# Kernel tuning notes

Hardware: AMD Instinct MI355X
Metric: run time of the kernel (lower is better)

The kernel has to match this reference:

```python
import jax, jax.numpy as jnp
import numpy as np

B, F, Q = 8192, 128, 64
H1, H2 = 256, 256
THRESHOLD = 0.95
EPS = 1e-12


def setup_inputs() -> dict:
    key = jax.random.key(0)
    ks = jax.random.split(key, 8)
    in_dim = F + 1 + Q  # raw + quantum + graph feature
    def lin(k, fan_in, fan_out):
        bound = 1.0 / np.sqrt(fan_in)
        kw, kb = jax.random.split(k)
        W = jax.random.uniform(kw, (fan_out, fan_in), jnp.float32, -bound, bound)
        b = jax.random.uniform(kb, (fan_out,), jnp.float32, -bound, bound)
        return W, b
    W1, b1 = lin(ks[2], in_dim, H1)
    W2, b2 = lin(ks[3], H1, H2)
    W3, b3 = lin(ks[4], H2, 1)
    return {
        'x': jax.random.normal(ks[0], (B, F), jnp.float32),
        'quantum_features': jax.random.normal(ks[1], (B, Q), jnp.float32),
        'W1': W1, 'b1': b1, 'W2': W2, 'b2': b2, 'W3': W3, 'b3': b3,
    }


def _graph_feat(x):
    # normalized Gram matrix -> squared cosine fidelity -> threshold -> row mean
    xn = x / (jnp.linalg.norm(x, axis=1, keepdims=True) + EPS)  # [B, F]
    fid = jnp.square(xn @ xn.T)                                  # [B, B]
    adj = jnp.where(fid >= THRESHOLD, 1.0, 0.0)
    adj = adj * (1.0 - jnp.eye(x.shape[0], dtype=x.dtype))       # no self-edges
    return jnp.mean(adj, axis=1, keepdims=True)                  # [B, 1]


def reference(x, quantum_features, W1, b1, W2, b2, W3, b3):
    graph_feat = jax.lax.stop_gradient(_graph_feat(x))  # built under no_grad in torch
    feats = jnp.concatenate([x, quantum_features, graph_feat], axis=1)  # [B, F+Q+1]
    h = jax.nn.relu(feats @ W1.T + b1)
    h = jax.nn.relu(h @ W2.T + b2)
    out = h @ W3.T + b3  # [B, 1]
    return out[:, 0]
```

## Files before the change

kernel.cpp:

```cpp
#include <hip/hip_runtime.h>
#include <hip/hip_bf16.h>

typedef __attribute__((ext_vector_type(8))) short bf16x8;
typedef __attribute__((ext_vector_type(8))) int i32x8;
typedef __attribute__((ext_vector_type(4))) float f32x4;
typedef unsigned int uint;

#define NROWS 8192
#define F_DIM 128
#define Q_DIM 64
#define KPAD  224
#define H_DIM 256

static __device__ inline unsigned short bf_bits(__hip_bfloat16 b) {
  unsigned short u; __builtin_memcpy(&u, &b, 2); return u;
}
static __device__ inline uint packhl(float v) {
  __hip_bfloat16 h = __float2bfloat16(v);
  float hf = __bfloat162float(h);
  __hip_bfloat16 l = __float2bfloat16(v - hf);
  return ((uint)bf_bits(l) << 16) | (uint)bf_bits(h);
}

__global__ __launch_bounds__(256) void norm_prep_kernel(const float* __restrict__ x,
                                                        const float* __restrict__ q,
                                                        const float* __restrict__ W1,
                                                        const float* __restrict__ W2,
                                                        unsigned char* __restrict__ xn8,
                                                        uint* __restrict__ feats_p,
                                                        uint* __restrict__ W1P,
                                                        uint* __restrict__ W2P,
                                                        int* __restrict__ cnt) {
  int tid = threadIdx.x;
  if (blockIdx.x >= 2048) {
    int b = blockIdx.x - 2048;
    if (b < 256) {
      if (tid < KPAD) W1P[b * KPAD + tid] = (tid < 193) ? packhl(W1[b * 193 + tid]) : 0u;
    } else {
      int n = b - 256;
      W2P[n * 256 + tid] = packhl(W2[n * 256 + tid]);
    }
    return;
  }
  int lane = tid & 63;
  int row = blockIdx.x * 4 + (tid >> 6);
  if (blockIdx.x < 32) cnt[blockIdx.x * 256 + tid] = 0;
  const float2 v = *(const float2*)(x + (size_t)row * F_DIM + lane * 2);
  float s = v.x * v.x + v.y * v.y;
#pragma unroll
  for (int off = 32; off; off >>= 1) s += __shfl_xor(s, off);
  float inv = 1.0f / (sqrtf(s) + 1e-12f);
  int pk = __builtin_amdgcn_cvt_pk_fp8_f32(v.x * inv, v.y * inv, 0, 0);
  *(unsigned short*)(xn8 + (size_t)row * F_DIM + lane * 2) = (unsigned short)(pk & 0xffff);

  uint* frow = feats_p + (size_t)row * KPAD;
  uint2 u;
  u.x = packhl(v.x); u.y = packhl(v.y);
  *(uint2*)(frow + lane * 2) = u;
  if (lane < 32) {
    const float2 qv = *(const float2*)(q + (size_t)row * Q_DIM + lane * 2);
    u.x = packhl(qv.x); u.y = packhl(qv.y);
    *(uint2*)(frow + 128 + lane * 2) = u;
  } else if (lane < 48) {
    uint2 z = {0u, 0u};
    *(uint2*)(frow + 192 + (lane - 32) * 2) = z;
  }
}

__global__ __launch_bounds__(256) void gram8_kernel(const unsigned char* __restrict__ xn8,
                                                    int* __restrict__ cnt) {
  __shared__ char smem[32768];
  int tid = threadIdx.x;
  int lane = tid & 63;
  int wave = tid >> 6;
  int lr = lane & 15;
  int quad = lane >> 4;

  int t = blockIdx.x;
  int bi = (int)((129.0f - sqrtf(129.0f * 129.0f - 8.0f * (float)t)) * 0.5f);
  while ((bi + 1) * (129 - (bi + 1)) / 2 <= t) bi++;
  while (bi * (129 - bi) / 2 > t) bi--;
  int bj = bi + (t - bi * (129 - bi) / 2);
  int i0 = bi * 128, j0 = bj * 128;

#pragma unroll
  for (int it = 0; it < 8; ++it) {
    int half = it >> 2;
    int row = (it & 3) * 32 + (tid >> 3);
    int chunk = tid & 7;
    int grow = (half ? j0 : i0) + row;
    uint4 v = *(const uint4*)(xn8 + (size_t)grow * F_DIM + chunk * 16);
    *(uint4*)(smem + half * 16384 + row * 128 + ((chunk ^ (row & 7)) << 4)) = v;
  }
  __syncthreads();

  int wi = (wave >> 1) * 64, wj = (wave & 1) * 64;

  f32x4 acc[4][4];
#pragma unroll
  for (int i = 0; i < 4; i++)
#pragma unroll
    for (int j = 0; j < 4; j++) acc[i][j] = (f32x4){0.f, 0.f, 0.f, 0.f};

  i32x8 a[4], b[4];
#pragma unroll
  for (int tt = 0; tt < 4; tt++) {
    int r = wi + tt * 16 + lr;
    const char* base = smem + r * 128;
    uint4 lo = *(const uint4*)(base + (((2 * quad) ^ (r & 7)) << 4));
    uint4 hi = *(const uint4*)(base + (((2 * quad + 1) ^ (r & 7)) << 4));
    i32x8 f;
    f[0] = lo.x; f[1] = lo.y; f[2] = lo.z; f[3] = lo.w;
    f[4] = hi.x; f[5] = hi.y; f[6] = hi.z; f[7] = hi.w;
    a[tt] = f;
  }
#pragma unroll
  for (int tt = 0; tt < 4; tt++) {
    int r = wj + tt * 16 + lr;
    const char* base = smem + 16384 + r * 128;
    uint4 lo = *(const uint4*)(base + (((2 * quad) ^ (r & 7)) << 4));
    uint4 hi = *(const uint4*)(base + (((2 * quad + 1) ^ (r & 7)) << 4));
    i32x8 f;
    f[0] = lo.x; f[1] = lo.y; f[2] = lo.z; f[3] = lo.w;
    f[4] = hi.x; f[5] = hi.y; f[6] = hi.z; f[7] = hi.w;
    b[tt] = f;
  }

#pragma unroll
  for (int tr = 0; tr < 4; tr++)
#pragma unroll
    for (int tc = 0; tc < 4; tc++)
      acc[tr][tc] = __builtin_amdgcn_mfma_scale_f32_16x16x128_f8f6f4(
          a[tr], b[tc], acc[tr][tc], 0, 0, 0, 0x7f7f7f7f, 0, 0x7f7f7f7f);

  int i_base = i0 + wi, j_base = j0 + wj;
  bool diag_wave = (i_base == j_base);
  bool offdiag_block = (bi != bj);

  float mx = 0.f;
#pragma unroll
  for (int tr = 0; tr < 4; tr++)
#pragma unroll
    for (int tc = 0; tc < 4; tc++)
#pragma unroll
      for (int r = 0; r < 4; r++) {
        float v = acc[tr][tc][r];
        if (diag_wave && tr == tc && lr == quad * 4 + r) v = 0.f;
        mx = fmaxf(mx, fabsf(v));
      }
  if (__any(mx >= 0.9746f)) {
    for (int tr = 0; tr < 4; tr++)
      for (int tc = 0; tc < 4; tc++)
        for (int r = 0; r < 4; r++) {
          float v = acc[tr][tc][r];
          int row = i_base + tr * 16 + quad * 4 + r;
          int col = j_base + tc * 16 + lr;
          if (v * v >= 0.95f && row != col) {
            atomicAdd(&cnt[row], 1);
            if (offdiag_block) atomicAdd(&cnt[col], 1);
          }
        }
  }
}

template <int K, int MODE>
__global__ __launch_bounds__(256) void gemm_mfma(const uint* __restrict__ A,
                                                 const uint* __restrict__ Bp,
                                                 const float* __restrict__ bias,
                                                 uint* __restrict__ Out,
                                                 const float* __restrict__ W3,
                                                 const float* __restrict__ b3,
                                                 const int* __restrict__ cnt,
                                                 float* __restrict__ out) {
  __shared__ short Ahi[128 * 40];
  __shared__ short Alo[128 * 40];
  __shared__ short Bhi[64 * 40];
  __shared__ short Blo[64 * 40];

  int tid = threadIdx.x;
  int lane = tid & 63;
  int wave = tid >> 6;
  int lr = lane & 15;
  int quad = lane >> 4;
  int mb = blockIdx.x * 128;
  int nb = blockIdx.y * 64;
  int wm = (wave & 1) * 64;
  int wn = (wave >> 1) * 32;

  int a_row = tid >> 3;
  int a_c4 = (tid & 7) * 4;

  uint gf[4];
  if (MODE == 1 && a_c4 == 0) {
#pragma unroll
    for (int i = 0; i < 4; i++)
      gf[i] = packhl((float)cnt[mb + a_row + i * 32] * (1.0f / 8192.0f));
  }

  f32x4 acc[4][2];
#pragma unroll
  for (int i = 0; i < 4; i++)
#pragma unroll
    for (int j = 0; j < 2; j++) acc[i][j] = (f32x4){0.f, 0.f, 0.f, 0.f};

  constexpr int NIT = K / 32;
  uint4 ar[4], br[2];

#pragma unroll
  for (int i = 0; i < 4; i++)
    ar[i] = *(const uint4*)(A + (size_t)(mb + a_row + i * 32) * K + a_c4);
#pragma unroll
  for (int i = 0; i < 2; i++)
    br[i] = *(const uint4*)(Bp + (size_t)(nb + a_row + i * 32) * K + a_c4);

  for (int it = 0; it < NIT; ++it) {
    if (MODE == 1 && it == 6 && a_c4 == 0) {
#pragma unroll
      for (int i = 0; i < 4; i++) ar[i].x = gf[i];
    }
    __syncthreads();
#pragma unroll
    for (int i = 0; i < 4; i++) {
      int r = a_row + i * 32;
      uint h01 = (ar[i].x & 0xffffu) | (ar[i].y << 16);
      uint h23 = (ar[i].z & 0xffffu) | (ar[i].w << 16);
      uint l01 = (ar[i].x >> 16) | (ar[i].y & 0xffff0000u);
      uint l23 = (ar[i].z >> 16) | (ar[i].w & 0xffff0000u);
      *(uint2*)&Ahi[r * 40 + a_c4] = (uint2){h01, h23};
      *(uint2*)&Alo[r * 40 + a_c4] = (uint2){l01, l23};
    }
#pragma unroll
    for (int i = 0; i < 2; i++) {
      int r = a_row + i * 32;
      uint h01 = (br[i].x & 0xffffu) | (br[i].y << 16);
      uint h23 = (br[i].z & 0xffffu) | (br[i].w << 16);
      uint l01 = (br[i].x >> 16) | (br[i].y & 0xffff0000u);
      uint l23 = (br[i].z >> 16) | (br[i].w & 0xffff0000u);
      *(uint2*)&Bhi[r * 40 + a_c4] = (uint2){h01, h23};
      *(uint2*)&Blo[r * 40 + a_c4] = (uint2){l01, l23};
    }
    __syncthreads();

    if (it + 1 < NIT) {
      int k0 = (it + 1) * 32;
#pragma unroll
      for (int i = 0; i < 4; i++)
        ar[i] = *(const uint4*)(A + (size_t)(mb + a_row + i * 32) * K + k0 + a_c4);
#pragma unroll
      for (int i = 0; i < 2; i++)
        br[i] = *(const uint4*)(Bp + (size_t)(nb + a_row + i * 32) * K + k0 + a_c4);
    }

    bf16x8 ahi[4], alo[4], bhi[2], blo[2];
#pragma unroll
    for (int tt = 0; tt < 4; tt++) {
      int r = wm + tt * 16 + lr;
      ahi[tt] = *(const bf16x8*)&Ahi[r * 40 + quad * 8];
      alo[tt] = *(const bf16x8*)&Alo[r * 40 + quad * 8];
    }
#pragma unroll
    for (int tc = 0; tc < 2; tc++) {
      int r = wn + tc * 16 + lr;
      bhi[tc] = *(const bf16x8*)&Bhi[r * 40 + quad * 8];
      blo[tc] = *(const bf16x8*)&Blo[r * 40 + quad * 8];
    }
#pragma unroll
    for (int tt = 0; tt < 4; tt++)
#pragma unroll
      for (int tc = 0; tc < 2; tc++) {
        acc[tt][tc] = __builtin_amdgcn_mfma_f32_16x16x32_bf16(ahi[tt], bhi[tc], acc[tt][tc], 0, 0, 0);
        acc[tt][tc] = __builtin_amdgcn_mfma_f32_16x16x32_bf16(ahi[tt], blo[tc], acc[tt][tc], 0, 0, 0);
        acc[tt][tc] = __builtin_amdgcn_mfma_f32_16x16x32_bf16(alo[tt], bhi[tc], acc[tt][tc], 0, 0, 0);
      }
  }

  if (MODE == 1) {
#pragma unroll
    for (int tc = 0; tc < 2; tc++) {
      int n = nb + wn + tc * 16 + lr;
      float bv = bias[n];
#pragma unroll
      for (int tt = 0; tt < 4; tt++) {
        int m0 = mb + wm + tt * 16 + quad * 4;
#pragma unroll
        for (int r = 0; r < 4; r++) {
          float v = fmaxf(acc[tt][tc][r] + bv, 0.f);
          Out[(size_t)(m0 + r) * 256 + n] = packhl(v);
        }
      }
    }
  } else {
    float b3v = (blockIdx.y == 0 && wn == 0) ? b3[0] : 0.f;
#pragma unroll
    for (int tt = 0; tt < 4; tt++) {
      float s[4] = {0.f, 0.f, 0.f, 0.f};
#pragma unroll
      for (int tc = 0; tc < 2; tc++) {
        int n = nb + wn + tc * 16 + lr;
        float bv = bias[n];
        float w3v = W3[n];
#pragma unroll
        for (int r = 0; r < 4; r++) {
          float v = fmaxf(acc[tt][tc][r] + bv, 0.f);
          s[r] += v * w3v;
        }
      }
#pragma unroll
      for (int r = 0; r < 4; r++) {
        s[r] += __shfl_xor(s[r], 1);
        s[r] += __shfl_xor(s[r], 2);
        s[r] += __shfl_xor(s[r], 4);
        s[r] += __shfl_xor(s[r], 8);
      }
      if (lr == 0) {
        int m0 = mb + wm + tt * 16 + quad * 4;
#pragma unroll
        for (int r = 0; r < 4; r++) atomicAdd(&out[m0 + r], s[r] + b3v);
      }
    }
  }
}

extern "C" void kernel_launch(void* const* d_in, const int* in_sizes, int n_in,
                              void* d_out, int out_size, void* d_ws, size_t ws_size,
                              hipStream_t stream) {
  const float* x  = (const float*)d_in[0];
  const float* q  = (const float*)d_in[1];
  const float* W1 = (const float*)d_in[2];
  const float* b1 = (const float*)d_in[3];
  const float* W2 = (const float*)d_in[4];
  const float* b2 = (const float*)d_in[5];
  const float* W3 = (const float*)d_in[6];
  const float* b3 = (const float*)d_in[7];
  float* out = (float*)d_out;

  char* ws = (char*)d_ws;
  unsigned char* xn8 = (unsigned char*)(ws);
  int*  cnt     = (int*)(ws + 0x100000);
  uint* W1P     = (uint*)(ws + 0x110000);
  uint* W2P     = (uint*)(ws + 0x150000);
  uint* feats_p = (uint*)(ws + 0x190000);
  uint* h1p     = (uint*)(ws + 0x890000);

  hipMemsetAsync(d_out, 0, (size_t)out_size * 4, stream);
  norm_prep_kernel<<<dim3(2560), dim3(256), 0, stream>>>(x, q, W1, W2, xn8, feats_p, W1P, W2P, cnt);
  gram8_kernel<<<dim3(2080), dim3(256), 0, stream>>>(xn8, cnt);
  gemm_mfma<KPAD, 1><<<dim3(64, 4), dim3(256), 0, stream>>>(feats_p, W1P, b1, h1p, nullptr, nullptr, cnt, nullptr);
  gemm_mfma<256, 2><<<dim3(64, 4), dim3(256), 0, stream>>>(h1p, W2P, b2, nullptr, W3, b3, nullptr, out);
}
```

Baseline: 103.8 us.

## Split hi/lo bf16 planes and load MFMA fragments directly from global memory

Stores the bf16 hi/lo split of features and weights as separate planar arrays instead of interleaved pairs. The GEMMs and the Gram kernel can then load MFMA operands straight from global memory without LDS staging, repacking or barriers. The GEMM tile shrinks to 64x64 with a doubled grid, and the output memset is folded into the prep kernel to drop one launch. In exchange, operand reuse now relies on L1/L2 instead of shared memory, and the GEMM loads are strided per row.

```diff
diff --git a/kernel.cpp b/kernel.cpp
--- a/kernel.cpp
+++ b/kernel.cpp
@@ -15,11 +15,11 @@
 static __device__ inline unsigned short bf_bits(__hip_bfloat16 b) {
   unsigned short u; __builtin_memcpy(&u, &b, 2); return u;
 }
-static __device__ inline uint packhl(float v) {
-  __hip_bfloat16 h = __float2bfloat16(v);
-  float hf = __bfloat162float(h);
-  __hip_bfloat16 l = __float2bfloat16(v - hf);
-  return ((uint)bf_bits(l) << 16) | (uint)bf_bits(h);
+static __device__ inline void split_hl(float v, unsigned short& h, unsigned short& l) {
+  __hip_bfloat16 hb = __float2bfloat16(v);
+  float hf = __bfloat162float(hb);
+  __hip_bfloat16 lb = __float2bfloat16(v - hf);
+  h = bf_bits(hb); l = bf_bits(lb);
 }
 
 __global__ __launch_bounds__(256) void norm_prep_kernel(const float* __restrict__ x,
@@ -27,24 +27,39 @@
                                                         const float* __restrict__ W1,
                                                         const float* __restrict__ W2,
                                                         unsigned char* __restrict__ xn8,
-                                                        uint* __restrict__ feats_p,
-                                                        uint* __restrict__ W1P,
-                                                        uint* __restrict__ W2P,
-                                                        int* __restrict__ cnt) {
+                                                        unsigned short* __restrict__ fh,
+                                                        unsigned short* __restrict__ fl,
+                                                        unsigned short* __restrict__ w1h,
+                                                        unsigned short* __restrict__ w1l,
+                                                        unsigned short* __restrict__ w2h,
+                                                        unsigned short* __restrict__ w2l,
+                                                        int* __restrict__ cnt,
+                                                        float* __restrict__ out) {
   int tid = threadIdx.x;
   if (blockIdx.x >= 2048) {
     int b = blockIdx.x - 2048;
     if (b < 256) {
-      if (tid < KPAD) W1P[b * KPAD + tid] = (tid < 193) ? packhl(W1[b * 193 + tid]) : 0u;
+      if (tid < KPAD) {
+        unsigned short h = 0, l = 0;
+        if (tid < 193) split_hl(W1[b * 193 + tid], h, l);
+        w1h[b * KPAD + tid] = h;
+        w1l[b * KPAD + tid] = l;
+      }
     } else {
       int n = b - 256;
-      W2P[n * 256 + tid] = packhl(W2[n * 256 + tid]);
+      unsigned short h, l;
+      split_hl(W2[n * 256 + tid], h, l);
+      w2h[n * 256 + tid] = h;
+      w2l[n * 256 + tid] = l;
     }
     return;
   }
   int lane = tid & 63;
   int row = blockIdx.x * 4 + (tid >> 6);
-  if (blockIdx.x < 32) cnt[blockIdx.x * 256 + tid] = 0;
+  if (blockIdx.x < 32) {
+    cnt[blockIdx.x * 256 + tid] = 0;
+    out[blockIdx.x * 256 + tid] = 0.f;
+  }
   const float2 v = *(const float2*)(x + (size_t)row * F_DIM + lane * 2);
   float s = v.x * v.x + v.y * v.y;
 #pragma unroll
@@ -53,23 +68,25 @@
   int pk = __builtin_amdgcn_cvt_pk_fp8_f32(v.x * inv, v.y * inv, 0, 0);
   *(unsigned short*)(xn8 + (size_t)row * F_DIM + lane * 2) = (unsigned short)(pk & 0xffff);
 
-  uint* frow = feats_p + (size_t)row * KPAD;
-  uint2 u;
-  u.x = packhl(v.x); u.y = packhl(v.y);
-  *(uint2*)(frow + lane * 2) = u;
+  unsigned short h0, l0, h1, l1;
+  unsigned short* fhr = fh + (size_t)row * KPAD;
+  unsigned short* flr = fl + (size_t)row * KPAD;
+  split_hl(v.x, h0, l0); split_hl(v.y, h1, l1);
+  *(uint*)(fhr + lane * 2) = (uint)h0 | ((uint)h1 << 16);
+  *(uint*)(flr + lane * 2) = (uint)l0 | ((uint)l1 << 16);
   if (lane < 32) {
     const float2 qv = *(const float2*)(q + (size_t)row * Q_DIM + lane * 2);
-    u.x = packhl(qv.x); u.y = packhl(qv.y);
-    *(uint2*)(frow + 128 + lane * 2) = u;
+    split_hl(qv.x, h0, l0); split_hl(qv.y, h1, l1);
+    *(uint*)(fhr + 128 + lane * 2) = (uint)h0 | ((uint)h1 << 16);
+    *(uint*)(flr + 128 + lane * 2) = (uint)l0 | ((uint)l1 << 16);
   } else if (lane < 48) {
-    uint2 z = {0u, 0u};
-    *(uint2*)(frow + 192 + (lane - 32) * 2) = z;
+    *(uint*)(fhr + 192 + (lane - 32) * 2) = 0u;
+    *(uint*)(flr + 192 + (lane - 32) * 2) = 0u;
   }
 }
 
 __global__ __launch_bounds__(256) void gram8_kernel(const unsigned char* __restrict__ xn8,
                                                     int* __restrict__ cnt) {
-  __shared__ char smem[32768];
   int tid = threadIdx.x;
   int lane = tid & 63;
   int wave = tid >> 6;
@@ -81,34 +98,14 @@
   while ((bi + 1) * (129 - (bi + 1)) / 2 <= t) bi++;
   while (bi * (129 - bi) / 2 > t) bi--;
   int bj = bi + (t - bi * (129 - bi) / 2);
-  int i0 = bi * 128, j0 = bj * 128;
-
-#pragma unroll
-  for (int it = 0; it < 8; ++it) {
-    int half = it >> 2;
-    int row = (it & 3) * 32 + (tid >> 3);
-    int chunk = tid & 7;
-    int grow = (half ? j0 : i0) + row;
-    uint4 v = *(const uint4*)(xn8 + (size_t)grow * F_DIM + chunk * 16);
-    *(uint4*)(smem + half * 16384 + row * 128 + ((chunk ^ (row & 7)) << 4)) = v;
-  }
-  __syncthreads();
-
-  int wi = (wave >> 1) * 64, wj = (wave & 1) * 64;
-
-  f32x4 acc[4][4];
-#pragma unroll
-  for (int i = 0; i < 4; i++)
-#pragma unroll
-    for (int j = 0; j < 4; j++) acc[i][j] = (f32x4){0.f, 0.f, 0.f, 0.f};
+  int i_base = bi * 128 + (wave >> 1) * 64;
+  int j_base = bj * 128 + (wave & 1) * 64;
 
   i32x8 a[4], b[4];
 #pragma unroll
   for (int tt = 0; tt < 4; tt++) {
-    int r = wi + tt * 16 + lr;
-    const char* base = smem + r * 128;
-    uint4 lo = *(const uint4*)(base + (((2 * quad) ^ (r & 7)) << 4));
-    uint4 hi = *(const uint4*)(base + (((2 * quad + 1) ^ (r & 7)) << 4));
+    const uint4* p = (const uint4*)(xn8 + (size_t)(i_base + tt * 16 + lr) * F_DIM + quad * 32);
+    uint4 lo = p[0], hi = p[1];
     i32x8 f;
     f[0] = lo.x; f[1] = lo.y; f[2] = lo.z; f[3] = lo.w;
     f[4] = hi.x; f[5] = hi.y; f[6] = hi.z; f[7] = hi.w;
@@ -116,16 +113,20 @@
   }
 #pragma unroll
   for (int tt = 0; tt < 4; tt++) {
-    int r = wj + tt * 16 + lr;
-    const char* base = smem + 16384 + r * 128;
-    uint4 lo = *(const uint4*)(base + (((2 * quad) ^ (r & 7)) << 4));
-    uint4 hi = *(const uint4*)(base + (((2 * quad + 1) ^ (r & 7)) << 4));
+    const uint4* p = (const uint4*)(xn8 + (size_t)(j_base + tt * 16 + lr) * F_DIM + quad * 32);
+    uint4 lo = p[0], hi = p[1];
     i32x8 f;
     f[0] = lo.x; f[1] = lo.y; f[2] = lo.z; f[3] = lo.w;
     f[4] = hi.x; f[5] = hi.y; f[6] = hi.z; f[7] = hi.w;
     b[tt] = f;
   }
 
+  f32x4 acc[4][4];
+#pragma unroll
+  for (int i = 0; i < 4; i++)
+#pragma unroll
+    for (int j = 0; j < 4; j++) acc[i][j] = (f32x4){0.f, 0.f, 0.f, 0.f};
+
 #pragma unroll
   for (int tr = 0; tr < 4; tr++)
 #pragma unroll
@@ -133,7 +134,6 @@
       acc[tr][tc] = __builtin_amdgcn_mfma_scale_f32_16x16x128_f8f6f4(
           a[tr], b[tc], acc[tr][tc], 0, 0, 0, 0x7f7f7f7f, 0, 0x7f7f7f7f);
 
-  int i_base = i0 + wi, j_base = j0 + wj;
   bool diag_wave = (i_base == j_base);
   bool offdiag_block = (bi != bj);
 
@@ -164,114 +164,84 @@
 }
 
 template <int K, int MODE>
-__global__ __launch_bounds__(256) void gemm_mfma(const uint* __restrict__ A,
-                                                 const uint* __restrict__ Bp,
+__global__ __launch_bounds__(256) void gemm_mfma(const unsigned short* __restrict__ Ah,
+                                                 const unsigned short* __restrict__ Al,
+                                                 const unsigned short* __restrict__ Bh,
+                                                 const unsigned short* __restrict__ Bl,
                                                  const float* __restrict__ bias,
-                                                 uint* __restrict__ Out,
+                                                 unsigned short* __restrict__ Oh,
+                                                 unsigned short* __restrict__ Ol,
                                                  const float* __restrict__ W3,
                                                  const float* __restrict__ b3,
                                                  const int* __restrict__ cnt,
                                                  float* __restrict__ out) {
-  __shared__ short Ahi[128 * 40];
-  __shared__ short Alo[128 * 40];
-  __shared__ short Bhi[64 * 40];
-  __shared__ short Blo[64 * 40];
-
   int tid = threadIdx.x;
   int lane = tid & 63;
   int wave = tid >> 6;
   int lr = lane & 15;
   int quad = lane >> 4;
-  int mb = blockIdx.x * 128;
+  int mb = blockIdx.x * 64;
   int nb = blockIdx.y * 64;
-  int wm = (wave & 1) * 64;
+  int wm = (wave & 1) * 32;
   int wn = (wave >> 1) * 32;
 
-  int a_row = tid >> 3;
-  int a_c4 = (tid & 7) * 4;
-
-  uint gf[4];
-  if (MODE == 1 && a_c4 == 0) {
-#pragma unroll
-    for (int i = 0; i < 4; i++)
-      gf[i] = packhl((float)cnt[mb + a_row + i * 32] * (1.0f / 8192.0f));
-  }
-
-  f32x4 acc[4][2];
-#pragma unroll
-  for (int i = 0; i < 4; i++)
+  int rowA0 = mb + wm + lr, rowA1 = rowA0 + 16;
+  int rowB0 = nb + wn + lr, rowB1 = rowB0 + 16;
+  const unsigned short* pah0 = Ah + (size_t)rowA0 * K + quad * 8;
+  const unsigned short* pah1 = Ah + (size_t)rowA1 * K + quad * 8;
+  const unsigned short* pal0 = Al + (size_t)rowA0 * K + quad * 8;
+  const unsigned short* pal1 = Al + (size_t)rowA1 * K + quad * 8;
+  const unsigned short* pbh0 = Bh + (size_t)rowB0 * K + quad * 8;
+  const unsigned short* pbh1 = Bh + (size_t)rowB1 * K + quad * 8;
+  const unsigned short* pbl0 = Bl + (size_t)rowB0 * K + quad * 8;
+  const unsigned short* pbl1 = Bl + (size_t)rowB1 * K + quad * 8;
+
+  f32x4 acc[2][2];
+#pragma unroll
+  for (int i = 0; i < 2; i++)
 #pragma unroll
     for (int j = 0; j < 2; j++) acc[i][j] = (f32x4){0.f, 0.f, 0.f, 0.f};
 
   constexpr int NIT = K / 32;
-  uint4 ar[4], br[2];
-
-#pragma unroll
-  for (int i = 0; i < 4; i++)
-    ar[i] = *(const uint4*)(A + (size_t)(mb + a_row + i * 32) * K + a_c4);
-#pragma unroll
-  for (int i = 0; i < 2; i++)
-    br[i] = *(const uint4*)(Bp + (size_t)(nb + a_row + i * 32) * K + a_c4);
-
+  bf16x8 cah[2], cal[2], cbh[2], cbl[2];
+  cah[0] = *(const bf16x8*)(pah0); cah[1] = *(const bf16x8*)(pah1);
+  cal[0] = *(const bf16x8*)(pal0); cal[1] = *(const bf16x8*)(pal1);
+  cbh[0] = *(const bf16x8*)(pbh0); cbh[1] = *(const bf16x8*)(pbh1);
+  cbl[0] = *(const bf16x8*)(pbl0); cbl[1] = *(const bf16x8*)(pbl1);
+
+#pragma unroll
   for (int it = 0; it < NIT; ++it) {
-    if (MODE == 1 && it == 6 && a_c4 == 0) {
-#pragma unroll
-      for (int i = 0; i < 4; i++) ar[i].x = gf[i];
-    }
-    __syncthreads();
-#pragma unroll
-    for (int i = 0; i < 4; i++) {
-      int r = a_row + i * 32;
-      uint h01 = (ar[i].x & 0xffffu) | (ar[i].y << 16);
-      uint h23 = (ar[i].z & 0xffffu) | (ar[i].w << 16);
-      uint l01 = (ar[i].x >> 16) | (ar[i].y & 0xffff0000u);
-      uint l23 = (ar[i].z >> 16) | (ar[i].w & 0xffff0000u);
-      *(uint2*)&Ahi[r * 40 + a_c4] = (uint2){h01, h23};
-      *(uint2*)&Alo[r * 40 + a_c4] = (uint2){l01, l23};
-    }
+    bf16x8 nah[2], nal[2], nbh[2], nbl[2];
+    if (it + 1 < NIT) {
+      int o = (it + 1) * 32;
+      nah[0] = *(const bf16x8*)(pah0 + o); nah[1] = *(const bf16x8*)(pah1 + o);
+      nal[0] = *(const bf16x8*)(pal0 + o); nal[1] = *(const bf16x8*)(pal1 + o);
+      nbh[0] = *(const bf16x8*)(pbh0 + o); nbh[1] = *(const bf16x8*)(pbh1 + o);
+      nbl[0] = *(const bf16x8*)(pbl0 + o); nbl[1] = *(const bf16x8*)(pbl1 + o);
+    }
+    if (MODE == 1 && it == 6 && quad == 0) {
+#pragma unroll
+      for (int tt = 0; tt < 2; tt++) {
+        float g = (float)cnt[rowA0 + tt * 16] * (1.0f / 8192.0f);
+        unsigned short h, l;
+        split_hl(g, h, l);
+        cah[tt][0] = (short)h;
+        cal[tt][0] = (short)l;
+      }
+    }
+#pragma unroll
+    for (int tt = 0; tt < 2; tt++)
+#pragma unroll
+      for (int tc = 0; tc < 2; tc++) {
+        acc[tt][tc] = __builtin_amdgcn_mfma_f32_16x16x32_bf16(cah[tt], cbh[tc], acc[tt][tc], 0, 0, 0);
+        acc[tt][tc] = __builtin_amdgcn_mfma_f32_16x16x32_bf16(cah[tt], cbl[tc], acc[tt][tc], 0, 0, 0);
+        acc[tt][tc] = __builtin_amdgcn_mfma_f32_16x16x32_bf16(cal[tt], cbh[tc], acc[tt][tc], 0, 0, 0);
+      }
 #pragma unroll
     for (int i = 0; i < 2; i++) {
-      int r = a_row + i * 32;
-      uint h01 = (br[i].x & 0xffffu) | (br[i].y << 16);
-      uint h23 = (br[i].z & 0xffffu) | (br[i].w << 16);
-      uint l01 = (br[i].x >> 16) | (br[i].y & 0xffff0000u);
-      uint l23 = (br[i].z >> 16) | (br[i].w & 0xffff0000u);
-      *(uint2*)&Bhi[r * 40 + a_c4] = (uint2){h01, h23};
-      *(uint2*)&Blo[r * 40 + a_c4] = (uint2){l01, l23};
-    }
-    __syncthreads();
-
-    if (it + 1 < NIT) {
-      int k0 = (it + 1) * 32;
-#pragma unroll
-      for (int i = 0; i < 4; i++)
-        ar[i] = *(const uint4*)(A + (size_t)(mb + a_row + i * 32) * K + k0 + a_c4);
-#pragma unroll
-      for (int i = 0; i < 2; i++)
-        br[i] = *(const uint4*)(Bp + (size_t)(nb + a_row + i * 32) * K + k0 + a_c4);
-    }
-
-    bf16x8 ahi[4], alo[4], bhi[2], blo[2];
-#pragma unroll
-    for (int tt = 0; tt < 4; tt++) {
-      int r = wm + tt * 16 + lr;
-      ahi[tt] = *(const bf16x8*)&Ahi[r * 40 + quad * 8];
-      alo[tt] = *(const bf16x8*)&Alo[r * 40 + quad * 8];
-    }
-#pragma unroll
-    for (int tc = 0; tc < 2; tc++) {
-      int r = wn + tc * 16 + lr;
-      bhi[tc] = *(const bf16x8*)&Bhi[r * 40 + quad * 8];
-      blo[tc] = *(const bf16x8*)&Blo[r * 40 + quad * 8];
-    }
-#pragma unroll
-    for (int tt = 0; tt < 4; tt++)
-#pragma unroll
-      for (int tc = 0; tc < 2; tc++) {
-        acc[tt][tc] = __builtin_amdgcn_mfma_f32_16x16x32_bf16(ahi[tt], bhi[tc], acc[tt][tc], 0, 0, 0);
-        acc[tt][tc] = __builtin_amdgcn_mfma_f32_16x16x32_bf16(ahi[tt], blo[tc], acc[tt][tc], 0, 0, 0);
-        acc[tt][tc] = __builtin_amdgcn_mfma_f32_16x16x32_bf16(alo[tt], bhi[tc], acc[tt][tc], 0, 0, 0);
-      }
+      cah[i] = nah[i]; cal[i] = nal[i];
+      cbh[i] = nbh[i]; cbl[i] = nbl[i];
+    }
   }
 
   if (MODE == 1) {
@@ -280,19 +250,22 @@
       int n = nb + wn + tc * 16 + lr;
       float bv = bias[n];
 #pragma unroll
-      for (int tt = 0; tt < 4; tt++) {
+      for (int tt = 0; tt < 2; tt++) {
         int m0 = mb + wm + tt * 16 + quad * 4;
 #pragma unroll
         for (int r = 0; r < 4; r++) {
           float v = fmaxf(acc[tt][tc][r] + bv, 0.f);
-          Out[(size_t)(m0 + r) * 256 + n] = packhl(v);
+          unsigned short h, l;
+          split_hl(v, h, l);
+          Oh[(size_t)(m0 + r) * 256 + n] = h;
+          Ol[(size_t)(m0 + r) * 256 + n] = l;
         }
       }
     }
   } else {
     float b3v = (blockIdx.y == 0 && wn == 0) ? b3[0] : 0.f;
 #pragma unroll
-    for (int tt = 0; tt < 4; tt++) {
+    for (int tt = 0; tt < 2; tt++) {
       float s[4] = {0.f, 0.f, 0.f, 0.f};
 #pragma unroll
       for (int tc = 0; tc < 2; tc++) {
@@ -335,16 +308,22 @@
   float* out = (float*)d_out;
 
   char* ws = (char*)d_ws;
-  unsigned char* xn8 = (unsigned char*)(ws);
-  int*  cnt     = (int*)(ws + 0x100000);
-  uint* W1P     = (uint*)(ws + 0x110000);
-  uint* W2P     = (uint*)(ws + 0x150000);
-  uint* feats_p = (uint*)(ws + 0x190000);
-  uint* h1p     = (uint*)(ws + 0x890000);
-
-  hipMemsetAsync(d_out, 0, (size_t)out_size * 4, stream);
-  norm_prep_kernel<<<dim3(2560), dim3(256), 0, stream>>>(x, q, W1, W2, xn8, feats_p, W1P, W2P, cnt);
+  unsigned char*  xn8 = (unsigned char*)(ws);
+  int*            cnt = (int*)(ws + 0x100000);
+  unsigned short* fh  = (unsigned short*)(ws + 0x110000);
+  unsigned short* fl  = (unsigned short*)(ws + 0x500000);
+  unsigned short* w1h = (unsigned short*)(ws + 0x8F0000);
+  unsigned short* w1l = (unsigned short*)(ws + 0x910000);
+  unsigned short* w2h = (unsigned short*)(ws + 0x930000);
+  unsigned short* w2l = (unsigned short*)(ws + 0x950000);
+  unsigned short* h1h = (unsigned short*)(ws + 0x970000);
+  unsigned short* h1l = (unsigned short*)(ws + 0xD70000);
+
+  norm_prep_kernel<<<dim3(2560), dim3(256), 0, stream>>>(x, q, W1, W2, xn8, fh, fl,
+                                                         w1h, w1l, w2h, w2l, cnt, out);
   gram8_kernel<<<dim3(2080), dim3(256), 0, stream>>>(xn8, cnt);
-  gemm_mfma<KPAD, 1><<<dim3(64, 4), dim3(256), 0, stream>>>(feats_p, W1P, b1, h1p, nullptr, nullptr, cnt, nullptr);
-  gemm_mfma<256, 2><<<dim3(64, 4), dim3(256), 0, stream>>>(h1p, W2P, b2, nullptr, W3, b3, nullptr, out);
-}
+  gemm_mfma<KPAD, 1><<<dim3(128, 4), dim3(256), 0, stream>>>(fh, fl, w1h, w1l, b1,
+                                                             h1h, h1l, nullptr, nullptr, cnt, nullptr);
+  gemm_mfma<256, 2><<<dim3(128, 4), dim3(256), 0, stream>>>(h1h, h1l, w2h, w2l, b2,
+                                                            nullptr, nullptr, W3, b3, nullptr, out);
+}
```

Result: slower. 120.2 us (+15.8%).

## Fuse both MLP GEMMs and W3 reduction into one kernel keeping H1 in LDS

Applied to the files above, without the earlier changes.

Replaces the two separate split-bf16 GEMM launches with a single fused MLP kernel. Each block of 32 rows builds its input features directly from x, q and cnt in shared memory, computes H1 into a swizzled LDS buffer, then runs the second GEMM and the W3 dot product in place. This drops the packed feats and h1 global buffers, the output memset, the atomics and one launch. In exchange each block streams the full W1P and W2P weights and the grid shrinks to 256 blocks, which may lower occupancy and parallelism.

```diff
diff --git a/kernel.cpp b/kernel.cpp
--- a/kernel.cpp
+++ b/kernel.cpp
@@ -21,13 +21,19 @@
   __hip_bfloat16 l = __float2bfloat16(v - hf);
   return ((uint)bf_bits(l) << 16) | (uint)bf_bits(h);
 }
+static __device__ inline void split_hl(float v, unsigned short& h, unsigned short& l) {
+  __hip_bfloat16 hb = __float2bfloat16(v);
+  float hf = __bfloat162float(hb);
+  __hip_bfloat16 lb = __float2bfloat16(v - hf);
+  h = bf_bits(hb); l = bf_bits(lb);
+}
+
+union uu { uint4 u; bf16x8 v; };
 
 __global__ __launch_bounds__(256) void norm_prep_kernel(const float* __restrict__ x,
-                                                        const float* __restrict__ q,
                                                         const float* __restrict__ W1,
                                                         const float* __restrict__ W2,
                                                         unsigned char* __restrict__ xn8,
-                                                        uint* __restrict__ feats_p,
                                                         uint* __restrict__ W1P,
                                                         uint* __restrict__ W2P,
                                                         int* __restrict__ cnt) {
@@ -52,19 +58,6 @@
   float inv = 1.0f / (sqrtf(s) + 1e-12f);
   int pk = __builtin_amdgcn_cvt_pk_fp8_f32(v.x * inv, v.y * inv, 0, 0);
   *(unsigned short*)(xn8 + (size_t)row * F_DIM + lane * 2) = (unsigned short)(pk & 0xffff);
-
-  uint* frow = feats_p + (size_t)row * KPAD;
-  uint2 u;
-  u.x = packhl(v.x); u.y = packhl(v.y);
-  *(uint2*)(frow + lane * 2) = u;
-  if (lane < 32) {
-    const float2 qv = *(const float2*)(q + (size_t)row * Q_DIM + lane * 2);
-    u.x = packhl(qv.x); u.y = packhl(qv.y);
-    *(uint2*)(frow + 128 + lane * 2) = u;
-  } else if (lane < 48) {
-    uint2 z = {0u, 0u};
-    *(uint2*)(frow + 192 + (lane - 32) * 2) = z;
-  }
 }
 
 __global__ __launch_bounds__(256) void gram8_kernel(const unsigned char* __restrict__ xn8,
@@ -163,162 +156,209 @@
   }
 }
 
-template <int K, int MODE>
-__global__ __launch_bounds__(256) void gemm_mfma(const uint* __restrict__ A,
-                                                 const uint* __restrict__ Bp,
-                                                 const float* __restrict__ bias,
-                                                 uint* __restrict__ Out,
-                                                 const float* __restrict__ W3,
-                                                 const float* __restrict__ b3,
-                                                 const int* __restrict__ cnt,
-                                                 float* __restrict__ out) {
-  __shared__ short Ahi[128 * 40];
-  __shared__ short Alo[128 * 40];
-  __shared__ short Bhi[64 * 40];
-  __shared__ short Blo[64 * 40];
+__global__ __launch_bounds__(256) void fused_mlp_kernel(const float* __restrict__ x,
+                                                        const float* __restrict__ q,
+                                                        const uint* __restrict__ W1P,
+                                                        const uint* __restrict__ W2P,
+                                                        const float* __restrict__ b1,
+                                                        const float* __restrict__ b2,
+                                                        const float* __restrict__ W3,
+                                                        const float* __restrict__ b3,
+                                                        const int* __restrict__ cnt,
+                                                        float* __restrict__ out) {
+  __shared__ char smem[65536];
+  short* Ahs = (short*)smem;
+  short* Als = (short*)(smem + 14848);
+  uint*  H1  = (uint*)smem;
+  uint*  Bx  = (uint*)(smem + 32768);
+  float* part = (float*)(smem + 32768);
 
   int tid = threadIdx.x;
   int lane = tid & 63;
-  int wave = tid >> 6;
+  int wv = tid >> 6;
   int lr = lane & 15;
   int quad = lane >> 4;
-  int mb = blockIdx.x * 128;
-  int nb = blockIdx.y * 64;
-  int wm = (wave & 1) * 64;
-  int wn = (wave >> 1) * 32;
-
-  int a_row = tid >> 3;
-  int a_c4 = (tid & 7) * 4;
-
-  uint gf[4];
-  if (MODE == 1 && a_c4 == 0) {
-#pragma unroll
-    for (int i = 0; i < 4; i++)
-      gf[i] = packhl((float)cnt[mb + a_row + i * 32] * (1.0f / 8192.0f));
-  }
-
-  f32x4 acc[4][2];
-#pragma unroll
-  for (int i = 0; i < 4; i++)
-#pragma unroll
-    for (int j = 0; j < 2; j++) acc[i][j] = (f32x4){0.f, 0.f, 0.f, 0.f};
-
-  constexpr int NIT = K / 32;
-  uint4 ar[4], br[2];
-
-#pragma unroll
-  for (int i = 0; i < 4; i++)
-    ar[i] = *(const uint4*)(A + (size_t)(mb + a_row + i * 32) * K + a_c4);
+  int mb = blockIdx.x * 32;
+
+  {
+    int r = tid >> 3;
+    int c8 = (tid & 7) * 4;
+#pragma unroll
+    for (int it = 0; it < 7; ++it) {
+      int col = it * 32 + c8;
+      float4 v = {0.f, 0.f, 0.f, 0.f};
+      if (it < 4)      v = *(const float4*)(x + (size_t)(mb + r) * F_DIM + col);
+      else if (it < 6) v = *(const float4*)(q + (size_t)(mb + r) * Q_DIM + (col - 128));
+      else if (c8 == 0) v.x = (float)cnt[mb + r] * (1.0f / 8192.0f);
+      unsigned short h0, l0, h1, l1, h2, l2, h3, l3;
+      split_hl(v.x, h0, l0); split_hl(v.y, h1, l1);
+      split_hl(v.z, h2, l2); split_hl(v.w, h3, l3);
+      *(uint2*)&Ahs[r * 232 + col] = (uint2){(uint)h0 | ((uint)h1 << 16), (uint)h2 | ((uint)h3 << 16)};
+      *(uint2*)&Als[r * 232 + col] = (uint2){(uint)l0 | ((uint)l1 << 16), (uint)l2 | ((uint)l3 << 16)};
+    }
+  }
+
+  f32x4 acc[2][4];
 #pragma unroll
   for (int i = 0; i < 2; i++)
-    br[i] = *(const uint4*)(Bp + (size_t)(nb + a_row + i * 32) * K + a_c4);
-
-  for (int it = 0; it < NIT; ++it) {
-    if (MODE == 1 && it == 6 && a_c4 == 0) {
-#pragma unroll
-      for (int i = 0; i < 4; i++) ar[i].x = gf[i];
-    }
+#pragma unroll
+    for (int j = 0; j < 4; j++) acc[i][j] = (f32x4){0.f, 0.f, 0.f, 0.f};
+
+  for (int kc = 0; kc < 7; ++kc) {
+    int k0 = kc * 32;
     __syncthreads();
 #pragma unroll
-    for (int i = 0; i < 4; i++) {
-      int r = a_row + i * 32;
-      uint h01 = (ar[i].x & 0xffffu) | (ar[i].y << 16);
-      uint h23 = (ar[i].z & 0xffffu) | (ar[i].w << 16);
-      uint l01 = (ar[i].x >> 16) | (ar[i].y & 0xffff0000u);
-      uint l23 = (ar[i].z >> 16) | (ar[i].w & 0xffff0000u);
-      *(uint2*)&Ahi[r * 40 + a_c4] = (uint2){h01, h23};
-      *(uint2*)&Alo[r * 40 + a_c4] = (uint2){l01, l23};
-    }
-#pragma unroll
-    for (int i = 0; i < 2; i++) {
-      int r = a_row + i * 32;
-      uint h01 = (br[i].x & 0xffffu) | (br[i].y << 16);
-      uint h23 = (br[i].z & 0xffffu) | (br[i].w << 16);
-      uint l01 = (br[i].x >> 16) | (br[i].y & 0xffff0000u);
-      uint l23 = (br[i].z >> 16) | (br[i].w & 0xffff0000u);
-      *(uint2*)&Bhi[r * 40 + a_c4] = (uint2){h01, h23};
-      *(uint2*)&Blo[r * 40 + a_c4] = (uint2){l01, l23};
+    for (int i = 0; i < 8; ++i) {
+      int flat = i * 256 + tid;
+      int n = flat >> 3, j = flat & 7;
+      uint4 w = *(const uint4*)(W1P + (size_t)n * KPAD + k0 + j * 4);
+      *(uint4*)&Bx[n * 32 + ((j ^ (n & 7)) * 4)] = w;
     }
     __syncthreads();
-
-    if (it + 1 < NIT) {
-      int k0 = (it + 1) * 32;
-#pragma unroll
-      for (int i = 0; i < 4; i++)
-        ar[i] = *(const uint4*)(A + (size_t)(mb + a_row + i * 32) * K + k0 + a_c4);
-#pragma unroll
-      for (int i = 0; i < 2; i++)
-        br[i] = *(const uint4*)(Bp + (size_t)(nb + a_row + i * 32) * K + k0 + a_c4);
-    }
-
-    bf16x8 ahi[4], alo[4], bhi[2], blo[2];
-#pragma unroll
-    for (int tt = 0; tt < 4; tt++) {
-      int r = wm + tt * 16 + lr;
-      ahi[tt] = *(const bf16x8*)&Ahi[r * 40 + quad * 8];
-      alo[tt] = *(const bf16x8*)&Alo[r * 40 + quad * 8];
-    }
-#pragma unroll
-    for (int tc = 0; tc < 2; tc++) {
-      int r = wn + tc * 16 + lr;
-      bhi[tc] = *(const bf16x8*)&Bhi[r * 40 + quad * 8];
-      blo[tc] = *(const bf16x8*)&Blo[r * 40 + quad * 8];
-    }
-#pragma unroll
-    for (int tt = 0; tt < 4; tt++)
-#pragma unroll
-      for (int tc = 0; tc < 2; tc++) {
-        acc[tt][tc] = __builtin_amdgcn_mfma_f32_16x16x32_bf16(ahi[tt], bhi[tc], acc[tt][tc], 0, 0, 0);
-        acc[tt][tc] = __builtin_amdgcn_mfma_f32_16x16x32_bf16(ahi[tt], blo[tc], acc[tt][tc], 0, 0, 0);
-        acc[tt][tc] = __builtin_amdgcn_mfma_f32_16x16x32_bf16(alo[tt], bhi[tc], acc[tt][tc], 0, 0, 0);
+    bf16x8 ah[2], al[2], bh[4], bl[4];
+#pragma unroll
+    for (int tt = 0; tt < 2; ++tt) {
+      int row = tt * 16 + lr;
+      ah[tt] = *(const bf16x8*)&Ahs[row * 232 + k0 + quad * 8];
+      al[tt] = *(const bf16x8*)&Als[row * 232 + k0 + quad * 8];
+    }
+#pragma unroll
+    for (int tc = 0; tc < 4; ++tc) {
+      int n = wv * 64 + tc * 16 + lr;
+      uint4 u0 = *(const uint4*)&Bx[n * 32 + (((quad * 2) ^ (n & 7)) * 4)];
+      uint4 u1 = *(const uint4*)&Bx[n * 32 + (((quad * 2 + 1) ^ (n & 7)) * 4)];
+      uu h, l;
+      h.u.x = (u0.x & 0xffffu) | (u0.y << 16);
+      h.u.y = (u0.z & 0xffffu) | (u0.w << 16);
+      h.u.z = (u1.x & 0xffffu) | (u1.y << 16);
+      h.u.w = (u1.z & 0xffffu) | (u1.w << 16);
+      l.u.x = (u0.x >> 16) | (u0.y & 0xffff0000u);
+      l.u.y = (u0.z >> 16) | (u0.w & 0xffff0000u);
+      l.u.z = (u1.x >> 16) | (u1.y & 0xffff0000u);
+      l.u.w = (u1.z >> 16) | (u1.w & 0xffff0000u);
+      bh[tc] = h.v; bl[tc] = l.v;
+    }
+#pragma unroll
+    for (int tt = 0; tt < 2; ++tt)
+#pragma unroll
+      for (int tc = 0; tc < 4; ++tc) {
+        acc[tt][tc] = __builtin_amdgcn_mfma_f32_16x16x32_bf16(ah[tt], bh[tc], acc[tt][tc], 0, 0, 0);
+        acc[tt][tc] = __builtin_amdgcn_mfma_f32_16x16x32_bf16(ah[tt], bl[tc], acc[tt][tc], 0, 0, 0);
+        acc[tt][tc] = __builtin_amdgcn_mfma_f32_16x16x32_bf16(al[tt], bh[tc], acc[tt][tc], 0, 0, 0);
       }
   }
 
-  if (MODE == 1) {
-#pragma unroll
-    for (int tc = 0; tc < 2; tc++) {
-      int n = nb + wn + tc * 16 + lr;
-      float bv = bias[n];
-#pragma unroll
-      for (int tt = 0; tt < 4; tt++) {
-        int m0 = mb + wm + tt * 16 + quad * 4;
-#pragma unroll
-        for (int r = 0; r < 4; r++) {
-          float v = fmaxf(acc[tt][tc][r] + bv, 0.f);
-          Out[(size_t)(m0 + r) * 256 + n] = packhl(v);
-        }
+  __syncthreads();
+#pragma unroll
+  for (int tc = 0; tc < 4; ++tc) {
+    int n = wv * 64 + tc * 16 + lr;
+    float bv = b1[n];
+    int g = n >> 2, jj = n & 3;
+#pragma unroll
+    for (int tt = 0; tt < 2; ++tt)
+#pragma unroll
+      for (int r = 0; r < 4; ++r) {
+        int row = tt * 16 + quad * 4 + r;
+        float v = fmaxf(acc[tt][tc][r] + bv, 0.f);
+        H1[row * 256 + ((g ^ (row & 31)) * 4 + jj)] = packhl(v);
       }
-    }
-  } else {
-    float b3v = (blockIdx.y == 0 && wn == 0) ? b3[0] : 0.f;
-#pragma unroll
-    for (int tt = 0; tt < 4; tt++) {
-      float s[4] = {0.f, 0.f, 0.f, 0.f};
-#pragma unroll
-      for (int tc = 0; tc < 2; tc++) {
-        int n = nb + wn + tc * 16 + lr;
-        float bv = bias[n];
-        float w3v = W3[n];
-#pragma unroll
-        for (int r = 0; r < 4; r++) {
-          float v = fmaxf(acc[tt][tc][r] + bv, 0.f);
-          s[r] += v * w3v;
-        }
+  }
+#pragma unroll
+  for (int i = 0; i < 2; i++)
+#pragma unroll
+    for (int j = 0; j < 4; j++) acc[i][j] = (f32x4){0.f, 0.f, 0.f, 0.f};
+
+  for (int kc = 0; kc < 8; ++kc) {
+    int k0 = kc * 32;
+    __syncthreads();
+#pragma unroll
+    for (int i = 0; i < 8; ++i) {
+      int flat = i * 256 + tid;
+      int n = flat >> 3, j = flat & 7;
+      uint4 w = *(const uint4*)(W2P + (size_t)n * 256 + k0 + j * 4);
+      *(uint4*)&Bx[n * 32 + ((j ^ (n & 7)) * 4)] = w;
+    }
+    __syncthreads();
+    bf16x8 ah[2], al[2], bh[4], bl[4];
+#pragma unroll
+    for (int tt = 0; tt < 2; ++tt) {
+      int row = tt * 16 + lr;
+      int cb = kc * 8 + quad * 2;
+      uint4 u0 = *(const uint4*)&H1[row * 256 + ((cb ^ (row & 31)) * 4)];
+      uint4 u1 = *(const uint4*)&H1[row * 256 + (((cb + 1) ^ (row & 31)) * 4)];
+      uu h, l;
+      h.u.x = (u0.x & 0xffffu) | (u0.y << 16);
+      h.u.y = (u0.z & 0xffffu) | (u0.w << 16);
+      h.u.z = (u1.x & 0xffffu) | (u1.y << 16);
+      h.u.w = (u1.z & 0xffffu) | (u1.w << 16);
+      l.u.x = (u0.x >> 16) | (u0.y & 0xffff0000u);
+      l.u.y = (u0.z >> 16) | (u0.w & 0xffff0000u);
+      l.u.z = (u1.x >> 16) | (u1.y & 0xffff0000u);
+      l.u.w = (u1.z >> 16) | (u1.w & 0xffff0000u);
+      ah[tt] = h.v; al[tt] = l.v;
+    }
+#pragma unroll
+    for (int tc = 0; tc < 4; ++tc) {
+      int n = wv * 64 + tc * 16 + lr;
+      uint4 u0 = *(const uint4*)&Bx[n * 32 + (((quad * 2) ^ (n & 7)) * 4)];
+      uint4 u1 = *(const uint4*)&Bx[n * 32 + (((quad * 2 + 1) ^ (n & 7)) * 4)];
+      uu h, l;
+      h.u.x = (u0.x & 0xffffu) | (u0.y << 16);
+      h.u.y = (u0.z & 0xffffu) | (u0.w << 16);
+      h.u.z = (u1.x & 0xffffu) | (u1.y << 16);
+      h.u.w = (u1.z & 0xffffu) | (u1.w << 16);
+      l.u.x = (u0.x >> 16) | (u0.y & 0xffff0000u);
+      l.u.y = (u0.z >> 16) | (u0.w & 0xffff0000u);
+      l.u.z = (u1.x >> 16) | (u1.y & 0xffff0000u);
+      l.u.w = (u1.z >> 16) | (u1.w & 0xffff0000u);
+      bh[tc] = h.v; bl[tc] = l.v;
+    }
+#pragma unroll
+    for (int tt = 0; tt < 2; ++tt)
+#pragma unroll
+      for (int tc = 0; tc < 4; ++tc) {
+        acc[tt][tc] = __builtin_amdgcn_mfma_f32_16x16x32_bf16(ah[tt], bh[tc], acc[tt][tc], 0, 0, 0);
+        acc[tt][tc] = __builtin_amdgcn_mfma_f32_16x16x32_bf16(ah[tt], bl[tc], acc[tt][tc], 0, 0, 0);
+        acc[tt][tc] = __builtin_amdgcn_mfma_f32_16x16x32_bf16(al[tt], bh[tc], acc[tt][tc], 0, 0, 0);
       }
-#pragma unroll
-      for (int r = 0; r < 4; r++) {
-        s[r] += __shfl_xor(s[r], 1);
-        s[r] += __shfl_xor(s[r], 2);
-        s[r] += __shfl_xor(s[r], 4);
-        s[r] += __shfl_xor(s[r], 8);
-      }
-      if (lr == 0) {
-        int m0 = mb + wm + tt * 16 + quad * 4;
-#pragma unroll
-        for (int r = 0; r < 4; r++) atomicAdd(&out[m0 + r], s[r] + b3v);
-      }
-    }
-  }
+  }
+
+  float s[2][4];
+#pragma unroll
+  for (int tt = 0; tt < 2; ++tt)
+#pragma unroll
+    for (int r = 0; r < 4; ++r) s[tt][r] = 0.f;
+#pragma unroll
+  for (int tc = 0; tc < 4; ++tc) {
+    int n = wv * 64 + tc * 16 + lr;
+    float bv = b2[n];
+    float w3 = W3[n];
+#pragma unroll
+    for (int tt = 0; tt < 2; ++tt)
+#pragma unroll
+      for (int r = 0; r < 4; ++r)
+        s[tt][r] += fmaxf(acc[tt][tc][r] + bv, 0.f) * w3;
+  }
+#pragma unroll
+  for (int tt = 0; tt < 2; ++tt)
+#pragma unroll
+    for (int r = 0; r < 4; ++r) {
+      s[tt][r] += __shfl_xor(s[tt][r], 1);
+      s[tt][r] += __shfl_xor(s[tt][r], 2);
+      s[tt][r] += __shfl_xor(s[tt][r], 4);
+      s[tt][r] += __shfl_xor(s[tt][r], 8);
+    }
+  __syncthreads();
+  if (lr == 0) {
+#pragma unroll
+    for (int tt = 0; tt < 2; ++tt)
+#pragma unroll
+      for (int r = 0; r < 4; ++r)
+        part[wv * 32 + tt * 16 + quad * 4 + r] = s[tt][r];
+  }
+  __syncthreads();
+  if (tid < 32)
+    out[mb + tid] = part[tid] + part[32 + tid] + part[64 + tid] + part[96 + tid] + b3[0];
 }
 
 extern "C" void kernel_launch(void* const* d_in, const int* in_sizes, int n_in,
@@ -336,15 +376,11 @@
 
   char* ws = (char*)d_ws;
   unsigned char* xn8 = (unsigned char*)(ws);
-  int*  cnt     = (int*)(ws + 0x100000);
-  uint* W1P     = (uint*)(ws + 0x110000);
-  uint* W2P     = (uint*)(ws + 0x150000);
-  uint* feats_p = (uint*)(ws + 0x190000);
-  uint* h1p     = (uint*)(ws + 0x890000);
-
-  hipMemsetAsync(d_out, 0, (size_t)out_size * 4, stream);
-  norm_prep_kernel<<<dim3(2560), dim3(256), 0, stream>>>(x, q, W1, W2, xn8, feats_p, W1P, W2P, cnt);
+  int*  cnt = (int*)(ws + 0x100000);
+  uint* W1P = (uint*)(ws + 0x110000);
+  uint* W2P = (uint*)(ws + 0x150000);
+
+  norm_prep_kernel<<<dim3(2560), dim3(256), 0, stream>>>(x, W1, W2, xn8, W1P, W2P, cnt);
   gram8_kernel<<<dim3(2080), dim3(256), 0, stream>>>(xn8, cnt);
-  gemm_mfma<KPAD, 1><<<dim3(64, 4), dim3(256), 0, stream>>>(feats_p, W1P, b1, h1p, nullptr, nullptr, cnt, nullptr);
-  gemm_mfma<256, 2><<<dim3(64, 4), dim3(256), 0, stream>>>(h1p, W2P, b2, nullptr, W3, b3, nullptr, out);
-}
+  fused_mlp_kernel<<<dim3(256), dim3(256), 0, stream>>>(x, q, W1P, W2P, b1, b2, W3, b3, cnt, out);
+}
```

New measurement: 98.68 us. -4.9%, faster.
